# Kernel optimization log

Hardware: AMD Instinct MI355X
Metric: run time of the kernel (lower is better)

Reference implementation:

```python
import jax, jax.numpy as jnp
import numpy as np

H = 256; B = 64; MAXF = 32; L = 50; S = 50
TAU = 1.0; BIAS = 0.0  # m_tau / m_bias (undefined in source; fixed constants)


def setup_inputs() -> dict:
    key = jax.random.key(0)
    ks = jax.random.split(key, 16)
    s = 1.0 / np.sqrt(H)
    return {
        "self_x": jax.random.normal(ks[0], (B, H), jnp.float32),
        "common_x": jax.random.normal(ks[1], (B, MAXF, S, H), jnp.float32),
        "common_time": jax.random.uniform(ks[2], (B, MAXF, S), jnp.float32),
        "friend_x": jax.random.normal(ks[3], (B, MAXF, L, H), jnp.float32),
        "Wih0": jax.random.normal(ks[4], (3 * H, H), jnp.float32) * s,
        "Whh0": jax.random.normal(ks[5], (3 * H, H), jnp.float32) * s,
        "bih0": jax.random.normal(ks[6], (3 * H,), jnp.float32) * s,
        "bhh0": jax.random.normal(ks[7], (3 * H,), jnp.float32) * s,
        "Wih1": jax.random.normal(ks[8], (3 * H, H), jnp.float32) * s,
        "Whh1": jax.random.normal(ks[9], (3 * H, H), jnp.float32) * s,
        "bih1": jax.random.normal(ks[10], (3 * H,), jnp.float32) * s,
        "bhh1": jax.random.normal(ks[11], (3 * H,), jnp.float32) * s,
        "Wf": jax.random.normal(ks[12], (H, 2 * H), jnp.float32) * s,   # m_linear_friend
        "Wb": jax.random.normal(ks[13], (H, H), jnp.float32) * s,       # m_linear_beta
        "friend_len": jax.random.randint(ks[14], (B, MAXF), 1, L + 1, jnp.int32),
        "friend_num": jax.random.randint(ks[15], (B,), 1, MAXF + 1, jnp.int32),
        "common_len": jax.random.randint(jax.random.fold_in(key, 99), (B, MAXF), 1, S + 1, jnp.int32),
    }


def _gru_layer(x, Wih, Whh, bih, bhh):
    # x: [N, L, H] -> outputs [N, L, H]; torch GRU gate math, zero init hidden
    def step(h, xt):
        gi = xt @ Wih.T + bih
        gh = h @ Whh.T + bhh
        ir, iz, inn = jnp.split(gi, 3, axis=-1)
        hr, hz, hn = jnp.split(gh, 3, axis=-1)
        r = jax.nn.sigmoid(ir + hr)
        z = jax.nn.sigmoid(iz + hz)
        n = jnp.tanh(inn + r * hn)
        h = (1.0 - z) * n + z * h
        return h, h
    h0 = jnp.zeros((x.shape[0], Whh.shape[1]), x.dtype)
    _, ys = jax.lax.scan(step, h0, jnp.swapaxes(x, 0, 1))
    return jnp.swapaxes(ys, 0, 1)


def reference(self_x, common_x, common_time, friend_x,
              Wih0, Whh0, bih0, bhh0, Wih1, Whh1, bih1, bhh1,
              Wf, Wb, friend_len, friend_num, common_len):
    # --- GRU over all (user, friend) sequences, flattened ---
    fx = friend_x.reshape(B * MAXF, L, H)
    fx = _gru_layer(fx, Wih0, Whh0, bih0, bhh0)
    fx = _gru_layer(fx, Wih1, Whh1, bih1, bhh1)
    fx = fx.reshape(B, MAXF, L, H)

    # mask invalid time steps, gather last valid hidden state per friend
    t_mask = (jnp.arange(L)[None, None, :] < friend_len[:, :, None])  # [B,MAXF,L]
    fx = fx * t_mask[..., None].astype(fx.dtype)
    last_idx = jnp.clip(friend_len - 1, 0, L - 1)
    friend_last = jnp.take_along_axis(fx, last_idx[:, :, None, None], axis=2)[:, :, 0, :]  # [B,MAXF,H]

    # repeat_interleave(self_x) equivalent in dense layout, concat, project
    self_rep = jnp.broadcast_to(self_x[:, None, :], (B, MAXF, H))
    sf = jnp.concatenate([self_rep, friend_last], axis=-1)  # [B,MAXF,2H]
    sf = jnp.einsum('bfk,hk->bfh', sf, Wf)                   # m_linear_friend

    # attention scores over common items: bmm + softplus
    proj_c = jnp.einsum('bfsh,gh->bfsg', common_x, Wb)       # m_linear_beta, g==H
    scores = jax.nn.softplus(jnp.einsum('bfsh,bfh->bfs', proj_c, sf))

    temporal = jnp.exp(-common_time / TAU + BIAS)
    c_mask = (jnp.arange(S)[None, None, :] < common_len[:, :, None]).astype(scores.dtype)
    tf = jnp.sum(scores * temporal * c_mask, axis=-1)        # [B,MAXF]

    # pad_sequence semantics: invalid friend slots are zero (logits and vectors)
    f_valid = (jnp.arange(MAXF)[None, :] < friend_num[:, None]).astype(tf.dtype)
    tf = tf * f_valid
    friend_last = friend_last * f_valid[..., None]

    w = jax.nn.softmax(tf, axis=-1)                          # over padded MAXF, as in source
    return jnp.sum(w[..., None] * friend_last, axis=1)       # [B,H]
```

## Files before the change

kernel.cpp:

```cpp
#include <hip/hip_runtime.h>
#include <hip/hip_bf16.h>
#include <stdint.h>

#define HD    256
#define LL    50
#define SS    50
#define NB    64
#define MAXF  32
#define NSEQ  2048
#define MB    32
#define NBLK  64
#define XP    264

typedef __attribute__((ext_vector_type(8)))  short bf16x8;
typedef __attribute__((ext_vector_type(16))) float f32x16;
typedef __attribute__((ext_vector_type(4)))  unsigned short u16x4;

__device__ __forceinline__ f32x16 mfma32(bf16x8 a, bf16x8 b, f32x16 c) {
    return __builtin_amdgcn_mfma_f32_32x32x16_bf16(a, b, c, 0, 0, 0);
}

__device__ __forceinline__ unsigned short f2bf_rne(float f) {
    union { float f; uint32_t u; } v; v.f = f;
    uint32_t u = v.u;
    uint32_t r = u + 0x7FFFu + ((u >> 16) & 1u);
    return (unsigned short)(r >> 16);
}
__device__ __forceinline__ float bf2f(unsigned short b) {
    union { float f; uint32_t u; } v; v.u = ((uint32_t)b) << 16;
    return v.f;
}

__global__ void pack_kernel(const float* __restrict__ Wih0, const float* __restrict__ Whh0,
                            const float* __restrict__ Wih1, const float* __restrict__ Whh1,
                            const float* __restrict__ Wf,
                            unsigned short* __restrict__ wpk,
                            float* __restrict__ WfT) {
    int idx = blockIdx.x * blockDim.x + threadIdx.x;
    const int TOTW = 1572864;
    if (idx < TOTW) {
        int j    = idx & 7;
        int lane = (idx >> 3) & 63;
        int fr   = (idx >> 9) % 12;
        int t2   = (idx >> 9) / 12;
        int ks   = t2 & 15;
        int m    = (t2 >> 4) & 1;
        int l    = (t2 >> 5) & 1;
        int wvv  = t2 >> 6;
        int gate = fr >> 2, sub = (fr >> 1) & 1, plane = fr & 1;
        const float* W = (l == 0) ? (m == 0 ? Wih0 : Whh0)
                                  : (m == 0 ? Wih1 : Whh1);
        int n = gate * 256 + wvv * 64 + sub * 32 + (lane & 31);
        int k = ks * 16 + (lane >> 5) * 8 + j;
        float v = W[n * HD + k];
        unsigned short hi = f2bf_rne(v);
        wpk[idx] = plane ? f2bf_rne(v - bf2f(hi)) : hi;
    } else {
        int idx2 = idx - TOTW;
        if (idx2 < 512 * 256) {
            int k = idx2 >> 8; int h = idx2 & 255;
            WfT[k * 256 + h] = Wf[h * 512 + k];
        }
    }
}

__global__ void sort_kernel(const int* __restrict__ flen, int* __restrict__ sid) {
    __shared__ int hist[64];
    __shared__ int offs[64];
    int tid = threadIdx.x;
    if (tid < 64) hist[tid] = 0;
    __syncthreads();
    for (int i = tid; i < NSEQ; i += blockDim.x) atomicAdd(&hist[flen[i]], 1);
    __syncthreads();
    if (tid == 0) {
        int acc = 0;
        for (int v = 1; v <= 50; v++) { offs[v] = acc; acc += hist[v]; }
    }
    __syncthreads();
    for (int i = tid; i < NSEQ; i += blockDim.x) {
        int pos = atomicAdd(&offs[flen[i]], 1);
        sid[pos] = i;
    }
}

__global__ __launch_bounds__(256) __attribute__((amdgpu_waves_per_eu(1, 1)))
void gru_kernel(const float* __restrict__ friend_x,
                const int* __restrict__ flen,
                const int* __restrict__ sid,
                const unsigned short* __restrict__ wpk,
                const float* __restrict__ bih0, const float* __restrict__ bhh0,
                const float* __restrict__ bih1, const float* __restrict__ bhh1,
                float* __restrict__ friend_last) {
    __shared__ __align__(16) unsigned short Xhi[MB][XP],  Xlo[MB][XP];
    __shared__ __align__(16) unsigned short H0hi[MB][XP], H0lo[MB][XP];
    __shared__ __align__(16) unsigned short H1hi[MB][XP], H1lo[MB][XP];
    __shared__ int sidS[MB], lenS[MB];

    const int tid  = threadIdx.x;
    const int g    = blockIdx.x;
    const int wv   = tid >> 6;
    const int lane = tid & 63;
    const int l31  = lane & 31;
    const int half = lane >> 5;

    if (tid < MB) {
        int s_ = sid[g * MB + tid];
        sidS[tid] = s_;
        lenS[tid] = flen[s_];
    }
    for (int i = tid; i < MB * XP / 2; i += 256) {
        ((uint32_t*)&H0hi[0][0])[i] = 0; ((uint32_t*)&H0lo[0][0])[i] = 0;
        ((uint32_t*)&H1hi[0][0])[i] = 0; ((uint32_t*)&H1lo[0][0])[i] = 0;
    }
    __syncthreads();

    int maxlen = 0;
#pragma unroll
    for (int s = 0; s < MB; s++) maxlen = max(maxlen, lenS[s]);

    const int j0 = wv * 64 + l31;

    float b0R[2], b0Z[2], b0Ni[2], b0Nh[2];
    float b1R[2], b1Z[2], b1Ni[2], b1Nh[2];
#pragma unroll
    for (int sub = 0; sub < 2; sub++) {
        int j = j0 + 32 * sub;
        b0R[sub]  = bih0[j] + bhh0[j];
        b0Z[sub]  = bih0[256 + j] + bhh0[256 + j];
        b0Ni[sub] = bih0[512 + j];
        b0Nh[sub] = bhh0[512 + j];
        b1R[sub]  = bih1[j] + bhh1[j];
        b1Z[sub]  = bih1[256 + j] + bhh1[256 + j];
        b1Ni[sub] = bih1[512 + j];
        b1Nh[sub] = bhh1[512 + j];
    }

    int srow[8];
#pragma unroll
    for (int r = 0; r < 8; r++) srow[r] = sidS[wv * 8 + r];

    float h0c[2][16], h1c[2][16];
#pragma unroll
    for (int sub = 0; sub < 2; sub++)
#pragma unroll
        for (int rg = 0; rg < 16; rg++) { h0c[sub][rg] = 0.f; h1c[sub][rg] = 0.f; }

    const int fragBase = l31 * XP + half * 8;

    auto loadB12 = [&](bf16x8* B, const unsigned short* p) {
#pragma unroll
        for (int f = 0; f < 12; f++) B[f] = *(const bf16x8*)(p + f * 512);
    };

    auto compute9 = [&](const bf16x8* B, bf16x8 ah, bf16x8 al,
                        f32x16* aR, f32x16* aZ, f32x16* aN) {
#pragma unroll
        for (int sub = 0; sub < 2; sub++) {
            aR[sub] = mfma32(ah, B[sub * 2],     aR[sub]);
            aR[sub] = mfma32(al, B[sub * 2],     aR[sub]);
            aR[sub] = mfma32(ah, B[sub * 2 + 1], aR[sub]);
            aZ[sub] = mfma32(ah, B[4 + sub * 2],     aZ[sub]);
            aZ[sub] = mfma32(al, B[4 + sub * 2],     aZ[sub]);
            aZ[sub] = mfma32(ah, B[4 + sub * 2 + 1], aZ[sub]);
            aN[sub] = mfma32(ah, B[8 + sub * 2],     aN[sub]);
            aN[sub] = mfma32(al, B[8 + sub * 2],     aN[sub]);
            aN[sub] = mfma32(ah, B[8 + sub * 2 + 1], aN[sub]);
        }
    };

    auto halfMM = [&](const unsigned short* pm,
                      const unsigned short* Ah_, const unsigned short* Al_,
                      f32x16* aR, f32x16* aZ, f32x16* aN) {
        bf16x8 B0[12], B1[12], ah0, al0, ah1, al1;
        loadB12(B0, pm);
        ah0 = *(const bf16x8*)(Ah_ + fragBase);
        al0 = *(const bf16x8*)(Al_ + fragBase);
        loadB12(B1, pm + 6144);
        ah1 = *(const bf16x8*)(Ah_ + fragBase + 16);
        al1 = *(const bf16x8*)(Al_ + fragBase + 16);
#pragma unroll 1
        for (int ks = 0; ks < 16; ks += 2) {
            compute9(B0, ah0, al0, aR, aZ, aN);
            if (ks + 2 < 16) {
                loadB12(B0, pm + (size_t)(ks + 2) * 6144);
                ah0 = *(const bf16x8*)(Ah_ + fragBase + (ks + 2) * 16);
                al0 = *(const bf16x8*)(Al_ + fragBase + (ks + 2) * 16);
            }
            compute9(B1, ah1, al1, aR, aZ, aN);
            if (ks + 3 < 16) {
                loadB12(B1, pm + (size_t)(ks + 3) * 6144);
                ah1 = *(const bf16x8*)(Ah_ + fragBase + (ks + 3) * 16);
                al1 = *(const bf16x8*)(Al_ + fragBase + (ks + 3) * 16);
            }
        }
    };

    auto initAcc = [&](f32x16* a, const float* b) {
#pragma unroll
        for (int sub = 0; sub < 2; sub++) {
            f32x16 v;
#pragma unroll
            for (int i = 0; i < 16; i++) v[i] = b[sub];
            a[sub] = v;
        }
    };

    auto epi = [&](f32x16* aR, f32x16* aZ, f32x16* aNi, f32x16* aNh,
                   float (*hc)[16],
                   unsigned short (*Ohi)[XP], unsigned short (*Olo)[XP],
                   bool gather, int t) {
#pragma unroll
        for (int sub = 0; sub < 2; sub++) {
            const int j = j0 + 32 * sub;
#pragma unroll
            for (int rg = 0; rg < 16; rg++) {
                const int row = (rg & 3) + ((rg >> 2) << 3) + (half << 2);
                float rr = 1.f / (1.f + __expf(-aR[sub][rg]));
                float zz = 1.f / (1.f + __expf(-aZ[sub][rg]));
                float nx = aNi[sub][rg] + rr * aNh[sub][rg];
                float e  = __expf(-2.f * fabsf(nx));
                float th = 1.f - 2.f * e / (1.f + e);
                th = (nx < 0.f) ? -th : th;
                float hNew = (1.f - zz) * th + zz * hc[sub][rg];
                hc[sub][rg] = hNew;
                unsigned short hi_ = f2bf_rne(hNew);
                Ohi[row][j] = hi_;
                Olo[row][j] = f2bf_rne(hNew - bf2f(hi_));
                if (gather && t == lenS[row] - 1)
                    friend_last[(size_t)sidS[row] * HD + j] = hNew;
            }
        }
    };

    auto stageWrite = [&](const float4* sx) {
#pragma unroll
        for (int r = 0; r < 8; r++) {
            int row = wv * 8 + r;
            float vals[4] = { sx[r].x, sx[r].y, sx[r].z, sx[r].w };
            u16x4 hi4, lo4;
#pragma unroll
            for (int e2 = 0; e2 < 4; e2++) {
                unsigned short h_ = f2bf_rne(vals[e2]);
                hi4[e2] = h_;
                lo4[e2] = f2bf_rne(vals[e2] - bf2f(h_));
            }
            *(u16x4*)&Xhi[row][lane * 4] = hi4;
            *(u16x4*)&Xlo[row][lane * 4] = lo4;
        }
    };

    {
        float4 sx[8];
#pragma unroll
        for (int r = 0; r < 8; r++)
            sx[r] = ((const float4*)(friend_x + ((size_t)srow[r] * LL) * HD))[lane];
        stageWrite(sx);
    }
    __syncthreads();

    const unsigned short* pw0 = wpk + (size_t)(wv * 2 + 0) * 196608 + (size_t)lane * 8;
    const unsigned short* pw1 = wpk + (size_t)(wv * 2 + 1) * 196608 + (size_t)lane * 8;

    for (int t = 0; t < maxlen; t++) {
        int tn = (t + 1 < maxlen) ? t + 1 : t;
        float4 sx[8];
#pragma unroll
        for (int r = 0; r < 8; r++)
            sx[r] = ((const float4*)(friend_x + ((size_t)srow[r] * LL + tn) * HD))[lane];

        f32x16 aR[2], aZ[2], aNi[2], aNh[2];
        initAcc(aR, b0R); initAcc(aZ, b0Z); initAcc(aNi, b0Ni); initAcc(aNh, b0Nh);
        halfMM(pw0,         &Xhi[0][0],  &Xlo[0][0],  aR, aZ, aNi);
        halfMM(pw0 + 98304, &H0hi[0][0], &H0lo[0][0], aR, aZ, aNh);
        __syncthreads();
        epi(aR, aZ, aNi, aNh, h0c, H0hi, H0lo, false, t);
        stageWrite(sx);
        __syncthreads();
        initAcc(aR, b1R); initAcc(aZ, b1Z); initAcc(aNi, b1Ni); initAcc(aNh, b1Nh);
        halfMM(pw1,         &H0hi[0][0], &H0lo[0][0], aR, aZ, aNi);
        halfMM(pw1 + 98304, &H1hi[0][0], &H1lo[0][0], aR, aZ, aNh);
        __syncthreads();
        epi(aR, aZ, aNi, aNh, h1c, H1hi, H1lo, true, t);
    }
}

__global__ __launch_bounds__(256)
void sfv_kernel(const float* __restrict__ self_x, const float* __restrict__ fl,
                const float* __restrict__ WfT, const float* __restrict__ Wb,
                float* __restrict__ vout) {
    __shared__ float S[256];
    __shared__ float T[256][33];
    int b = blockIdx.x, tid = threadIdx.x;
    S[tid] = self_x[b * 256 + tid];
    for (int i = tid; i < 32 * 256; i += 256) {
        int f = i >> 8, k = i & 255;
        T[k][f] = fl[((size_t)(b * 32 + f)) * 256 + k];
    }
    __syncthreads();
    float acc0 = 0.f;
    for (int k = 0; k < 256; k++) acc0 += WfT[k * 256 + tid] * S[k];
    float acc[32];
#pragma unroll
    for (int f = 0; f < 32; f++) acc[f] = acc0;
    for (int k = 0; k < 256; k++) {
        float w = WfT[(256 + k) * 256 + tid];
#pragma unroll
        for (int f = 0; f < 32; f++) acc[f] += w * T[k][f];
    }
    __syncthreads();
#pragma unroll
    for (int f = 0; f < 32; f++) T[tid][f] = acc[f];
    __syncthreads();
    float av[32];
#pragma unroll
    for (int f = 0; f < 32; f++) av[f] = 0.f;
    for (int gg = 0; gg < 256; gg++) {
        float w = Wb[gg * 256 + tid];
#pragma unroll
        for (int f = 0; f < 32; f++) av[f] += w * T[gg][f];
    }
#pragma unroll
    for (int f = 0; f < 32; f++)
        vout[((size_t)(b * 32 + f)) * 256 + tid] = av[f];
}

__global__ __launch_bounds__(256)
void tf_kernel(const float* __restrict__ common_x, const float* __restrict__ common_time,
               const int* __restrict__ clen, const float* __restrict__ v,
               float* __restrict__ tf) {
    __shared__ float V[256];
    __shared__ float partial[4];
    int n = blockIdx.x, tid = threadIdx.x, wv = tid >> 6, lane = tid & 63;
    V[tid] = v[(size_t)n * 256 + tid];
    __syncthreads();
    float4 vv = ((const float4*)V)[lane];
    int cl = clen[n];
    float acc = 0.f;
    for (int s = wv; s < SS; s += 4) {
        float4 cx = ((const float4*)(common_x + ((size_t)n * SS + s) * HD))[lane];
        float d = cx.x * vv.x + cx.y * vv.y + cx.z * vv.z + cx.w * vv.w;
#pragma unroll
        for (int off = 32; off; off >>= 1) d += __shfl_xor(d, off);
        if (lane == 0 && s < cl) {
            float sp = (d > 20.f) ? d : log1pf(__expf(d));
            acc += sp * __expf(-common_time[n * SS + s]);
        }
    }
    if (lane == 0) partial[wv] = acc;
    __syncthreads();
    if (tid == 0) tf[n] = partial[0] + partial[1] + partial[2] + partial[3];
}

__global__ __launch_bounds__(256)
void out_kernel(const float* __restrict__ tf, const int* __restrict__ fnum,
                const float* __restrict__ fl, float* __restrict__ out) {
    __shared__ float e[32];
    __shared__ float tfm[32];
    __shared__ float Zs;
    int b = blockIdx.x, tid = threadIdx.x;
    int nv = fnum[b];
    if (tid < 32) tfm[tid] = (tid < nv) ? tf[b * 32 + tid] : 0.f;
    __syncthreads();
    if (tid == 0) {
        float m = tfm[0];
        for (int f = 1; f < 32; f++) m = fmaxf(m, tfm[f]);
        float Z = 0.f;
        for (int f = 0; f < 32; f++) { e[f] = __expf(tfm[f] - m); Z += e[f]; }
        Zs = Z;
    }
    __syncthreads();
    float Zi = 1.f / Zs;
    float o = 0.f;
    for (int f = 0; f < nv; f++)
        o += e[f] * Zi * fl[((size_t)(b * 32 + f)) * 256 + tid];
    out[b * 256 + tid] = o;
}

extern "C" void kernel_launch(void* const* d_in, const int* in_sizes, int n_in,
                              void* d_out, int out_size, void* d_ws, size_t ws_size,
                              hipStream_t stream) {
    (void)in_sizes; (void)n_in; (void)out_size; (void)ws_size;
    const float* self_x      = (const float*)d_in[0];
    const float* common_x    = (const float*)d_in[1];
    const float* common_time = (const float*)d_in[2];
    const float* friend_x    = (const float*)d_in[3];
    const float* Wih0 = (const float*)d_in[4];
    const float* Whh0 = (const float*)d_in[5];
    const float* bih0 = (const float*)d_in[6];
    const float* bhh0 = (const float*)d_in[7];
    const float* Wih1 = (const float*)d_in[8];
    const float* Whh1 = (const float*)d_in[9];
    const float* bih1 = (const float*)d_in[10];
    const float* bhh1 = (const float*)d_in[11];
    const float* Wf   = (const float*)d_in[12];
    const float* Wb   = (const float*)d_in[13];
    const int* flen   = (const int*)d_in[14];
    const int* fnum   = (const int*)d_in[15];
    const int* clen   = (const int*)d_in[16];
    float* out = (float*)d_out;

    char* ws = (char*)d_ws;
    unsigned short* wpk = (unsigned short*)ws; ws += (size_t)1572864 * 2;
    float* WfT = (float*)ws;  ws += (size_t)512 * 256 * 4;
    int*   sid = (int*)ws;    ws += (size_t)2048 * 4;
    float* fl  = (float*)ws;  ws += (size_t)2048 * 256 * 4;
    float* vv  = (float*)ws;  ws += (size_t)2048 * 256 * 4;
    float* tf  = (float*)ws;  ws += (size_t)2048 * 4;

    pack_kernel<<<6656, 256, 0, stream>>>(Wih0, Whh0, Wih1, Whh1, Wf, wpk, WfT);
    sort_kernel<<<1, 256, 0, stream>>>(flen, sid);
    gru_kernel<<<NBLK, 256, 0, stream>>>(friend_x, flen, sid, wpk,
                                         bih0, bhh0, bih1, bhh1, fl);
    sfv_kernel<<<64, 256, 0, stream>>>(self_x, fl, WfT, Wb, vv);
    tf_kernel<<<2048, 256, 0, stream>>>(common_x, common_time, clen, vv, tf);
    out_kernel<<<64, 256, 0, stream>>>(tf, fnum, fl, out);
}
```

Before: 2.764 ms.

## Split GRU work across 8 waves per block with double-buffered input staging

The GRU kernel moves from 4 waves to 8 waves per block, and each wave now owns 32 hidden columns instead of 64. The packed weight layout is reordered to match. The input and recurrent matmuls of each layer are merged into one 32-step loop with a triple-buffered prefetch. The next timestep's input is double-buffered in shared memory and written during the layer-1 matmul, which removes that write from the layer-0 epilogue path. The aim is more latency hiding on the serial recurrence. In exchange, each wave's register budget halves and shared memory grows.

After: 6.673 ms. 2.41x slower.

```diff
diff --git a/kernel.cpp b/kernel.cpp
--- a/kernel.cpp
+++ b/kernel.cpp
@@ -14,6 +14,7 @@
 
 typedef __attribute__((ext_vector_type(8)))  short bf16x8;
 typedef __attribute__((ext_vector_type(16))) float f32x16;
+typedef __attribute__((ext_vector_type(4)))  float f32x4v;
 typedef __attribute__((ext_vector_type(4)))  unsigned short u16x4;
 
 __device__ __forceinline__ f32x16 mfma32(bf16x8 a, bf16x8 b, f32x16 c) {
@@ -39,18 +40,18 @@
     int idx = blockIdx.x * blockDim.x + threadIdx.x;
     const int TOTW = 1572864;
     if (idx < TOTW) {
-        int j    = idx & 7;
-        int lane = (idx >> 3) & 63;
-        int fr   = (idx >> 9) % 12;
-        int t2   = (idx >> 9) / 12;
-        int ks   = t2 & 15;
-        int m    = (t2 >> 4) & 1;
-        int l    = (t2 >> 5) & 1;
-        int wvv  = t2 >> 6;
-        int gate = fr >> 2, sub = (fr >> 1) & 1, plane = fr & 1;
+        int j     = idx & 7;
+        int lane  = (idx >> 3) & 63;
+        int plane = (idx >> 9) & 1;
+        int gate  = (idx >> 10) % 3;
+        int rest  = (idx >> 10) / 3;
+        int ks    = rest & 15;
+        int m     = (rest >> 4) & 1;
+        int l     = (rest >> 5) & 1;
+        int wvv   = rest >> 6;
         const float* W = (l == 0) ? (m == 0 ? Wih0 : Whh0)
                                   : (m == 0 ? Wih1 : Whh1);
-        int n = gate * 256 + wvv * 64 + sub * 32 + (lane & 31);
+        int n = gate * 256 + wvv * 32 + (lane & 31);
         int k = ks * 16 + (lane >> 5) * 8 + j;
         float v = W[n * HD + k];
         unsigned short hi = f2bf_rne(v);
@@ -83,7 +84,7 @@
     }
 }
 
-__global__ __launch_bounds__(256) __attribute__((amdgpu_waves_per_eu(1, 1)))
+__global__ __launch_bounds__(512) __attribute__((amdgpu_waves_per_eu(2, 2)))
 void gru_kernel(const float* __restrict__ friend_x,
                 const int* __restrict__ flen,
                 const int* __restrict__ sid,
@@ -91,9 +92,9 @@
                 const float* __restrict__ bih0, const float* __restrict__ bhh0,
                 const float* __restrict__ bih1, const float* __restrict__ bhh1,
                 float* __restrict__ friend_last) {
-    __shared__ __align__(16) unsigned short Xhi[MB][XP],  Xlo[MB][XP];
-    __shared__ __align__(16) unsigned short H0hi[MB][XP], H0lo[MB][XP];
-    __shared__ __align__(16) unsigned short H1hi[MB][XP], H1lo[MB][XP];
+    __shared__ __align__(16) unsigned short Xhi[2][MB][XP], Xlo[2][MB][XP];
+    __shared__ __align__(16) unsigned short H0hi[MB][XP],   H0lo[MB][XP];
+    __shared__ __align__(16) unsigned short H1hi[MB][XP],   H1lo[MB][XP];
     __shared__ int sidS[MB], lenS[MB];
 
     const int tid  = threadIdx.x;
@@ -108,7 +109,7 @@
         sidS[tid] = s_;
         lenS[tid] = flen[s_];
     }
-    for (int i = tid; i < MB * XP / 2; i += 256) {
+    for (int i = tid; i < MB * XP / 2; i += 512) {
         ((uint32_t*)&H0hi[0][0])[i] = 0; ((uint32_t*)&H0lo[0][0])[i] = 0;
         ((uint32_t*)&H1hi[0][0])[i] = 0; ((uint32_t*)&H1lo[0][0])[i] = 0;
     }
@@ -118,167 +119,135 @@
 #pragma unroll
     for (int s = 0; s < MB; s++) maxlen = max(maxlen, lenS[s]);
 
-    const int j0 = wv * 64 + l31;
-
-    float b0R[2], b0Z[2], b0Ni[2], b0Nh[2];
-    float b1R[2], b1Z[2], b1Ni[2], b1Nh[2];
-#pragma unroll
-    for (int sub = 0; sub < 2; sub++) {
-        int j = j0 + 32 * sub;
-        b0R[sub]  = bih0[j] + bhh0[j];
-        b0Z[sub]  = bih0[256 + j] + bhh0[256 + j];
-        b0Ni[sub] = bih0[512 + j];
-        b0Nh[sub] = bhh0[512 + j];
-        b1R[sub]  = bih1[j] + bhh1[j];
-        b1Z[sub]  = bih1[256 + j] + bhh1[256 + j];
-        b1Ni[sub] = bih1[512 + j];
-        b1Nh[sub] = bhh1[512 + j];
-    }
-
-    int srow[8];
-#pragma unroll
-    for (int r = 0; r < 8; r++) srow[r] = sidS[wv * 8 + r];
-
-    float h0c[2][16], h1c[2][16];
-#pragma unroll
-    for (int sub = 0; sub < 2; sub++)
-#pragma unroll
-        for (int rg = 0; rg < 16; rg++) { h0c[sub][rg] = 0.f; h1c[sub][rg] = 0.f; }
+    const int j = wv * 32 + l31;
+
+    const float b0R  = bih0[j] + bhh0[j];
+    const float b0Z  = bih0[256 + j] + bhh0[256 + j];
+    const float b0Ni = bih0[512 + j];
+    const float b0Nh = bhh0[512 + j];
+    const float b1R  = bih1[j] + bhh1[j];
+    const float b1Z  = bih1[256 + j] + bhh1[256 + j];
+    const float b1Ni = bih1[512 + j];
+    const float b1Nh = bhh1[512 + j];
+
+    int srow[4];
+#pragma unroll
+    for (int r = 0; r < 4; r++) srow[r] = sidS[wv * 4 + r];
+
+    float h0c[16], h1c[16];
+#pragma unroll
+    for (int rg = 0; rg < 16; rg++) { h0c[rg] = 0.f; h1c[rg] = 0.f; }
 
     const int fragBase = l31 * XP + half * 8;
-
-    auto loadB12 = [&](bf16x8* B, const unsigned short* p) {
-#pragma unroll
-        for (int f = 0; f < 12; f++) B[f] = *(const bf16x8*)(p + f * 512);
-    };
-
-    auto compute9 = [&](const bf16x8* B, bf16x8 ah, bf16x8 al,
-                        f32x16* aR, f32x16* aZ, f32x16* aN) {
-#pragma unroll
-        for (int sub = 0; sub < 2; sub++) {
-            aR[sub] = mfma32(ah, B[sub * 2],     aR[sub]);
-            aR[sub] = mfma32(al, B[sub * 2],     aR[sub]);
-            aR[sub] = mfma32(ah, B[sub * 2 + 1], aR[sub]);
-            aZ[sub] = mfma32(ah, B[4 + sub * 2],     aZ[sub]);
-            aZ[sub] = mfma32(al, B[4 + sub * 2],     aZ[sub]);
-            aZ[sub] = mfma32(ah, B[4 + sub * 2 + 1], aZ[sub]);
-            aN[sub] = mfma32(ah, B[8 + sub * 2],     aN[sub]);
-            aN[sub] = mfma32(al, B[8 + sub * 2],     aN[sub]);
-            aN[sub] = mfma32(ah, B[8 + sub * 2 + 1], aN[sub]);
-        }
-    };
-
-    auto halfMM = [&](const unsigned short* pm,
-                      const unsigned short* Ah_, const unsigned short* Al_,
-                      f32x16* aR, f32x16* aZ, f32x16* aN) {
-        bf16x8 B0[12], B1[12], ah0, al0, ah1, al1;
-        loadB12(B0, pm);
-        ah0 = *(const bf16x8*)(Ah_ + fragBase);
-        al0 = *(const bf16x8*)(Al_ + fragBase);
-        loadB12(B1, pm + 6144);
-        ah1 = *(const bf16x8*)(Ah_ + fragBase + 16);
-        al1 = *(const bf16x8*)(Al_ + fragBase + 16);
-#pragma unroll 1
-        for (int ks = 0; ks < 16; ks += 2) {
-            compute9(B0, ah0, al0, aR, aZ, aN);
-            if (ks + 2 < 16) {
-                loadB12(B0, pm + (size_t)(ks + 2) * 6144);
-                ah0 = *(const bf16x8*)(Ah_ + fragBase + (ks + 2) * 16);
-                al0 = *(const bf16x8*)(Al_ + fragBase + (ks + 2) * 16);
+    const unsigned short* wbase = wpk + (size_t)wv * 196608 + (size_t)lane * 8;
+
+    auto stageLoad = [&](int tsrc, f32x4v* sx) {
+#pragma unroll
+        for (int r = 0; r < 4; r++)
+            sx[r] = __builtin_nontemporal_load(
+                (const f32x4v*)(friend_x + ((size_t)srow[r] * LL + tsrc) * HD) + lane);
+    };
+    auto stageWrite = [&](int buf, const f32x4v* sx) {
+#pragma unroll
+        for (int r = 0; r < 4; r++) {
+            int row = wv * 4 + r;
+            u16x4 hi4, lo4;
+#pragma unroll
+            for (int e = 0; e < 4; e++) {
+                unsigned short h_ = f2bf_rne(sx[r][e]);
+                hi4[e] = h_;
+                lo4[e] = f2bf_rne(sx[r][e] - bf2f(h_));
             }
-            compute9(B1, ah1, al1, aR, aZ, aN);
-            if (ks + 3 < 16) {
-                loadB12(B1, pm + (size_t)(ks + 3) * 6144);
-                ah1 = *(const bf16x8*)(Ah_ + fragBase + (ks + 3) * 16);
-                al1 = *(const bf16x8*)(Al_ + fragBase + (ks + 3) * 16);
-            }
-        }
-    };
-
-    auto initAcc = [&](f32x16* a, const float* b) {
-#pragma unroll
-        for (int sub = 0; sub < 2; sub++) {
-            f32x16 v;
-#pragma unroll
-            for (int i = 0; i < 16; i++) v[i] = b[sub];
-            a[sub] = v;
-        }
-    };
-
-    auto epi = [&](f32x16* aR, f32x16* aZ, f32x16* aNi, f32x16* aNh,
-                   float (*hc)[16],
+            *(u16x4*)&Xhi[buf][row][lane * 4] = hi4;
+            *(u16x4*)&Xlo[buf][row][lane * 4] = lo4;
+        }
+    };
+
+    auto layerMM = [&](const unsigned short* pL,
+                       const unsigned short* A0h, const unsigned short* A0l,
+                       const unsigned short* A1h, const unsigned short* A1l,
+                       f32x16& aR, f32x16& aZ, f32x16& aNi, f32x16& aNh) {
+        bf16x8 B[3][6], ahb[3], alb[3];
+        auto pf = [&](int buf, int grp) {
+            const unsigned short* p = pL + (size_t)grp * 3072;
+#pragma unroll
+            for (int f = 0; f < 6; f++) B[buf][f] = *(const bf16x8*)(p + f * 512);
+            const unsigned short* Ah = (grp < 16) ? A0h : A1h;
+            const unsigned short* Al = (grp < 16) ? A0l : A1l;
+            int off = fragBase + (grp & 15) * 16;
+            ahb[buf] = *(const bf16x8*)(Ah + off);
+            alb[buf] = *(const bf16x8*)(Al + off);
+        };
+        pf(0, 0); pf(1, 1);
+#pragma unroll
+        for (int grp = 0; grp < 32; grp++) {
+            const int cur = grp % 3;
+            if (grp + 2 < 32) pf((grp + 2) % 3, grp + 2);
+            f32x16& aN = (grp < 16) ? aNi : aNh;
+            const bf16x8 ah = ahb[cur], al = alb[cur];
+            aR = mfma32(ah, B[cur][0], aR);
+            aR = mfma32(al, B[cur][0], aR);
+            aR = mfma32(ah, B[cur][1], aR);
+            aZ = mfma32(ah, B[cur][2], aZ);
+            aZ = mfma32(al, B[cur][2], aZ);
+            aZ = mfma32(ah, B[cur][3], aZ);
+            aN = mfma32(ah, B[cur][4], aN);
+            aN = mfma32(al, B[cur][4], aN);
+            aN = mfma32(ah, B[cur][5], aN);
+        }
+    };
+
+    auto initAcc = [&](f32x16& a, float b) {
+#pragma unroll
+        for (int i = 0; i < 16; i++) a[i] = b;
+    };
+
+    auto epi = [&](f32x16& aR, f32x16& aZ, f32x16& aNi, f32x16& aNh, float* hc,
                    unsigned short (*Ohi)[XP], unsigned short (*Olo)[XP],
                    bool gather, int t) {
 #pragma unroll
-        for (int sub = 0; sub < 2; sub++) {
-            const int j = j0 + 32 * sub;
-#pragma unroll
-            for (int rg = 0; rg < 16; rg++) {
-                const int row = (rg & 3) + ((rg >> 2) << 3) + (half << 2);
-                float rr = 1.f / (1.f + __expf(-aR[sub][rg]));
-                float zz = 1.f / (1.f + __expf(-aZ[sub][rg]));
-                float nx = aNi[sub][rg] + rr * aNh[sub][rg];
-                float e  = __expf(-2.f * fabsf(nx));
-                float th = 1.f - 2.f * e / (1.f + e);
-                th = (nx < 0.f) ? -th : th;
-                float hNew = (1.f - zz) * th + zz * hc[sub][rg];
-                hc[sub][rg] = hNew;
-                unsigned short hi_ = f2bf_rne(hNew);
-                Ohi[row][j] = hi_;
-                Olo[row][j] = f2bf_rne(hNew - bf2f(hi_));
-                if (gather && t == lenS[row] - 1)
-                    friend_last[(size_t)sidS[row] * HD + j] = hNew;
-            }
-        }
-    };
-
-    auto stageWrite = [&](const float4* sx) {
-#pragma unroll
-        for (int r = 0; r < 8; r++) {
-            int row = wv * 8 + r;
-            float vals[4] = { sx[r].x, sx[r].y, sx[r].z, sx[r].w };
-            u16x4 hi4, lo4;
-#pragma unroll
-            for (int e2 = 0; e2 < 4; e2++) {
-                unsigned short h_ = f2bf_rne(vals[e2]);
-                hi4[e2] = h_;
-                lo4[e2] = f2bf_rne(vals[e2] - bf2f(h_));
-            }
-            *(u16x4*)&Xhi[row][lane * 4] = hi4;
-            *(u16x4*)&Xlo[row][lane * 4] = lo4;
+        for (int rg = 0; rg < 16; rg++) {
+            const int row = (rg & 3) + ((rg >> 2) << 3) + (half << 2);
+            float rr = 1.f / (1.f + __expf(-aR[rg]));
+            float zz = 1.f / (1.f + __expf(-aZ[rg]));
+            float nx = aNi[rg] + rr * aNh[rg];
+            float e  = __expf(-2.f * fabsf(nx));
+            float th = 1.f - 2.f * e / (1.f + e);
+            th = (nx < 0.f) ? -th : th;
+            float hNew = (1.f - zz) * th + zz * hc[rg];
+            hc[rg] = hNew;
+            unsigned short hi_ = f2bf_rne(hNew);
+            Ohi[row][j] = hi_;
+            Olo[row][j] = f2bf_rne(hNew - bf2f(hi_));
+            if (gather && t == lenS[row] - 1)
+                __builtin_nontemporal_store(hNew, friend_last + (size_t)sidS[row] * HD + j);
         }
     };
 
     {
-        float4 sx[8];
-#pragma unroll
-        for (int r = 0; r < 8; r++)
-            sx[r] = ((const float4*)(friend_x + ((size_t)srow[r] * LL) * HD))[lane];
-        stageWrite(sx);
-    }
-    __syncthreads();
-
-    const unsigned short* pw0 = wpk + (size_t)(wv * 2 + 0) * 196608 + (size_t)lane * 8;
-    const unsigned short* pw1 = wpk + (size_t)(wv * 2 + 1) * 196608 + (size_t)lane * 8;
-
+        f32x4v sx[4];
+        stageLoad(0, sx);
+        stageWrite(0, sx);
+    }
+    __syncthreads();
+
+#pragma unroll 1
     for (int t = 0; t < maxlen; t++) {
-        int tn = (t + 1 < maxlen) ? t + 1 : t;
-        float4 sx[8];
-#pragma unroll
-        for (int r = 0; r < 8; r++)
-            sx[r] = ((const float4*)(friend_x + ((size_t)srow[r] * LL + tn) * HD))[lane];
-
-        f32x16 aR[2], aZ[2], aNi[2], aNh[2];
+        const int cb = t & 1, nb = cb ^ 1;
+        f32x16 aR, aZ, aNi, aNh;
         initAcc(aR, b0R); initAcc(aZ, b0Z); initAcc(aNi, b0Ni); initAcc(aNh, b0Nh);
-        halfMM(pw0,         &Xhi[0][0],  &Xlo[0][0],  aR, aZ, aNi);
-        halfMM(pw0 + 98304, &H0hi[0][0], &H0lo[0][0], aR, aZ, aNh);
+        layerMM(wbase, &Xhi[cb][0][0], &Xlo[cb][0][0], &H0hi[0][0], &H0lo[0][0],
+                aR, aZ, aNi, aNh);
         __syncthreads();
         epi(aR, aZ, aNi, aNh, h0c, H0hi, H0lo, false, t);
-        stageWrite(sx);
         __syncthreads();
+        int tn = (t + 1 < maxlen) ? t + 1 : t;
+        f32x4v sx[4];
+        stageLoad(tn, sx);
         initAcc(aR, b1R); initAcc(aZ, b1Z); initAcc(aNi, b1Ni); initAcc(aNh, b1Nh);
-        halfMM(pw1,         &H0hi[0][0], &H0lo[0][0], aR, aZ, aNi);
-        halfMM(pw1 + 98304, &H1hi[0][0], &H1lo[0][0], aR, aZ, aNh);
+        layerMM(wbase + 98304, &H0hi[0][0], &H0lo[0][0], &H1hi[0][0], &H1lo[0][0],
+                aR, aZ, aNi, aNh);
+        stageWrite(nb, sx);
         __syncthreads();
         epi(aR, aZ, aNi, aNh, h1c, H1hi, H1lo, true, t);
     }
@@ -409,7 +378,7 @@
 
     pack_kernel<<<6656, 256, 0, stream>>>(Wih0, Whh0, Wih1, Whh1, Wf, wpk, WfT);
     sort_kernel<<<1, 256, 0, stream>>>(flen, sid);
-    gru_kernel<<<NBLK, 256, 0, stream>>>(friend_x, flen, sid, wpk,
+    gru_kernel<<<NBLK, 512, 0, stream>>>(friend_x, flen, sid, wpk,
                                          bih0, bhh0, bih1, bhh1, fl);
     sfv_kernel<<<64, 256, 0, stream>>>(self_x, fl, WfT, Wb, vv);
     tf_kernel<<<2048, 256, 0, stream>>>(common_x, common_time, clen, vv, tf);
```
